# Kernel tuning notes

Hardware: AMD Instinct MI355X
Metric: run time of the kernel (lower is better)

## Reference

```python
import jax, jax.numpy as jnp
import numpy as np

B, S, D, H, L = 128, 200, 512, 512, 2  # batch, seq(=max_seq_len), input, hidden, layers


def _uni(key, shape, fan):
    bound = 1.0 / np.sqrt(fan)
    return jax.random.uniform(key, shape, jnp.float32, -bound, bound)


def setup_inputs() -> dict:
    key = jax.random.key(0)
    ks = jax.random.split(key, 12)
    x = jax.random.normal(ks[0], (B, S, D), jnp.float32)
    lens = jax.random.randint(ks[1], (B,), 1, S + 1).astype(jnp.int64)
    return {
        'x': x,
        'lens': lens,
        'Wih_f': _uni(ks[2], (L, 4 * H, D), H),
        'Whh_f': _uni(ks[3], (L, 4 * H, H), H),
        'bih_f': _uni(ks[4], (L, 4 * H), H),
        'bhh_f': _uni(ks[5], (L, 4 * H), H),
        'Wih_b': _uni(ks[6], (L, 4 * H, D), H),
        'Whh_b': _uni(ks[7], (L, 4 * H, H), H),
        'bih_b': _uni(ks[8], (L, 4 * H), H),
        'bhh_b': _uni(ks[9], (L, 4 * H), H),
    }


def _lstm_dir(xs, Wih, Whh, bih, bhh, reverse):
    # xs: [B,S,Din]. Precompute batched input projection, scan the recurrence.
    gx = jnp.einsum('bsd,gd->bsg', xs, Wih) + bih  # [B,S,4H]
    h0 = jnp.zeros((xs.shape[0], Whh.shape[1]), xs.dtype)
    c0 = jnp.zeros_like(h0)

    def step(carry, g_t):
        h, c = carry
        gates = g_t + h @ Whh.T + bhh
        i, f, g, o = jnp.split(gates, 4, axis=-1)  # PyTorch LSTMCell order
        i = jax.nn.sigmoid(i)
        f = jax.nn.sigmoid(f)
        g = jnp.tanh(g)
        o = jax.nn.sigmoid(o)
        c = f * c + i * g
        h = o * jnp.tanh(c)
        return (h, c), h

    _, hs = jax.lax.scan(step, (h0, c0), jnp.swapaxes(gx, 0, 1), reverse=reverse)
    return jnp.swapaxes(hs, 0, 1)  # [B,S,H], time-ordered


def reference(x, lens, Wih_f, Whh_f, bih_f, bhh_f, Wih_b, Whh_b, bih_b, bhh_b):
    valid = (jnp.arange(S)[None, :] < lens[:, None]).astype(x.dtype)[..., None]  # [B,S,1]
    f_in, b_in = x, x
    for l in range(L):
        f_h = _lstm_dir(f_in, Wih_f[l], Whh_f[l], bih_f[l], bhh_f[l], reverse=False)
        b_h = _lstm_dir(b_in, Wih_b[l], Whh_b[l], bih_b[l], bhh_b[l], reverse=True)
        f_h = f_h * valid  # masked_fill(mask, 0) for positions >= lens
        b_h = b_h * valid
        f_in, b_in = f_h, b_h
    return jnp.concatenate((f_in, b_in), axis=2)  # [B,S,2H]
```

## Files before the change

kernel.cpp:

```cpp
#include <hip/hip_runtime.h>
#include <hip/hip_bf16.h>

typedef __bf16 bf16x8 __attribute__((ext_vector_type(8)));
typedef _Float16 f16x8 __attribute__((ext_vector_type(8)));
typedef float f32x4 __attribute__((ext_vector_type(4)));

__device__ __forceinline__ unsigned short f2bf(float f) {
    unsigned int u = __builtin_bit_cast(unsigned int, f);
    u += 0x7FFFu + ((u >> 16) & 1u);
    return (unsigned short)(u >> 16);
}
__device__ __forceinline__ float bf2f(unsigned short s) {
    unsigned int u = ((unsigned int)s) << 16;
    return __builtin_bit_cast(float, u);
}

__device__ __forceinline__ void ldg_c(uint4& d, const void* p) {
    asm volatile("global_load_dwordx4 %0, %1, off sc0 sc1" : "=v"(d) : "v"(p));
}
__device__ __forceinline__ void stg_c32(void* p, unsigned v) {
    asm volatile("global_store_dword %0, %1, off sc0 sc1" :: "v"(p), "v"(v) : "memory");
}
__device__ __forceinline__ void vm_drain() {
    asm volatile("s_waitcnt vmcnt(0)" ::: "memory");
    __builtin_amdgcn_sched_barrier(0);
}
__device__ __forceinline__ void vm_wait_imm(int n) {
    switch (n) {
    case 0:  asm volatile("s_waitcnt vmcnt(0)"  ::: "memory"); break;
    case 4:  asm volatile("s_waitcnt vmcnt(4)"  ::: "memory"); break;
    case 8:  asm volatile("s_waitcnt vmcnt(8)"  ::: "memory"); break;
    case 12: asm volatile("s_waitcnt vmcnt(12)" ::: "memory"); break;
    case 16: asm volatile("s_waitcnt vmcnt(16)" ::: "memory"); break;
    case 20: asm volatile("s_waitcnt vmcnt(20)" ::: "memory"); break;
    case 24: asm volatile("s_waitcnt vmcnt(24)" ::: "memory"); break;
    default: asm volatile("s_waitcnt vmcnt(28)" ::: "memory"); break;
    }
    __builtin_amdgcn_sched_barrier(0);
}
__device__ __forceinline__ void lds_fence() {
    asm volatile("s_waitcnt lgkmcnt(0)" ::: "memory");
    __builtin_amdgcn_sched_barrier(0);
}

__device__ __forceinline__ void wait_flags(const unsigned* f, unsigned tgt) {
    int lane = threadIdx.x & 63;
    for (;;) {
        unsigned v = __hip_atomic_load(f + lane, __ATOMIC_RELAXED, __HIP_MEMORY_SCOPE_AGENT);
        if (__all((int)(v >= tgt))) break;
        __builtin_amdgcn_s_sleep(1);
    }
}

__global__ void prep_x(const float* __restrict__ x,
                       unsigned short* __restrict__ xh,
                       unsigned short* __restrict__ xl) {
    int g = blockIdx.x * 256 + threadIdx.x;
    if (g >= 1638400) return;
    int lane = g & 63;
    int kc   = (g >> 6) & 15;
    int nt   = (g >> 10) & 7;
    int t    = g >> 13;
    int batch = nt * 16 + (lane & 15);
    int k = kc * 32 + (lane >> 4) * 8;
    const float* s = x + ((size_t)batch * 200 + t) * 512 + k;
    float4 v0 = *(const float4*)s;
    float4 v1 = *(const float4*)(s + 4);
    float vv[8] = {v0.x, v0.y, v0.z, v0.w, v1.x, v1.y, v1.z, v1.w};
    unsigned int ph[4], pl[4];
    #pragma unroll
    for (int j = 0; j < 4; ++j) {
        float a = vv[2*j], b = vv[2*j+1];
        unsigned short ha = f2bf(a), hb = f2bf(b);
        unsigned short la = f2bf(a - bf2f(ha)), lb = f2bf(b - bf2f(hb));
        ph[j] = (unsigned)ha | ((unsigned)hb << 16);
        pl[j] = (unsigned)la | ((unsigned)lb << 16);
    }
    ((uint4*)xh)[g] = make_uint4(ph[0], ph[1], ph[2], ph[3]);
    ((uint4*)xl)[g] = make_uint4(pl[0], pl[1], pl[2], pl[3]);
}

__global__ void prep_w(const float* __restrict__ W,
                       unsigned short* __restrict__ wprep,
                       int dir, int isHH) {
    int g = blockIdx.x * 256 + threadIdx.x;
    if (g >= 262144) return;
    int lane = g & 63;
    int kc   = (g >> 6) & 15;
    int mt   = (g >> 10) & 1;
    int cu   = (g >> 11) & 63;
    int l    = g >> 17;
    int r = lane & 15;
    int grow = (2 * mt + (r >> 3)) * 512 + cu * 8 + (r & 7);
    int k = kc * 32 + (lane >> 4) * 8;
    const float* s = W + ((size_t)l * 2048 + grow) * 512 + k;
    float4 v0 = *(const float4*)s;
    float4 v1 = *(const float4*)(s + 4);
    float vv[8] = {v0.x, v0.y, v0.z, v0.w, v1.x, v1.y, v1.z, v1.w};
    bool f16fmt = isHH || (l == 1);
    unsigned int ph[4], pl[4];
    #pragma unroll
    for (int j = 0; j < 4; ++j) {
        float a = vv[2*j], b = vv[2*j+1];
        unsigned short ha, hb, la, lb;
        if (f16fmt) {
            _Float16 fa = (_Float16)a, fb = (_Float16)b;
            _Float16 ra = (_Float16)(a - (float)fa), rb = (_Float16)(b - (float)fb);
            ha = __builtin_bit_cast(unsigned short, fa);
            hb = __builtin_bit_cast(unsigned short, fb);
            la = __builtin_bit_cast(unsigned short, ra);
            lb = __builtin_bit_cast(unsigned short, rb);
        } else {
            ha = f2bf(a); hb = f2bf(b);
            la = f2bf(a - bf2f(ha)); lb = f2bf(b - bf2f(hb));
        }
        ph[j] = (unsigned)ha | ((unsigned)hb << 16);
        pl[j] = (unsigned)la | ((unsigned)lb << 16);
    }
    size_t blk = ((size_t)(dir * 2 + l) * 64 + cu) * 8192;
    size_t fH = blk + (size_t)((isHH * 2 + 0) * 2048 + mt * 1024 + kc * 64 + lane);
    size_t fL = blk + (size_t)((isHH * 2 + 1) * 2048 + mt * 1024 + kc * 64 + lane);
    ((uint4*)wprep)[fH] = make_uint4(ph[0], ph[1], ph[2], ph[3]);
    ((uint4*)wprep)[fL] = make_uint4(pl[0], pl[1], pl[2], pl[3]);
}

__global__ void bsum_k(const float* __restrict__ bih_f, const float* __restrict__ bhh_f,
                       const float* __restrict__ bih_b, const float* __restrict__ bhh_b,
                       float* __restrict__ bsum) {
    int i = blockIdx.x * 256 + threadIdx.x;
    if (i < 8192) {
        int dir = i >> 12, rem = i & 4095;
        const float* bi = dir ? bih_b : bih_f;
        const float* bh = dir ? bhh_b : bhh_f;
        bsum[i] = bi[rem] + bh[rem];
    }
}

__global__ void reset_k(uint4* __restrict__ p) {
    int g = blockIdx.x * 256 + threadIdx.x;
    if (g < 131136) p[g] = make_uint4(0, 0, 0, 0);
}

__global__ void __launch_bounds__(512)
lstm_persist(const unsigned short* __restrict__ xh,
             const unsigned short* __restrict__ xl,
             const unsigned short* __restrict__ wprep,
             const float*          __restrict__ bsum,
             unsigned short*       __restrict__ hbuf,
             const int*            __restrict__ lens,
             float*                __restrict__ dout,
             unsigned*             __restrict__ flagv)
{
    extern __shared__ char smem[];
    float* wexch  = (float*)(smem + 131072);
    float* cst    = (float*)(smem + 131072 + 17408);
    float* bias_l = (float*)(smem + 131072 + 17408 + 4224);

    const int bid  = blockIdx.x;
    const int xcd  = bid & 7;
    const int unit = xcd >> 1;
    const int slot = unit >> 1, dir = unit & 1;
    const int cu8  = ((xcd & 1) << 5) | (bid >> 3);
    const int hj0  = cu8 * 8;
    const int tid  = threadIdx.x;
    const int lane = tid & 63, ng = tid >> 6;
    const int l15  = lane & 15, kg = lane >> 4;
    const int wsel = dir * 2 + slot;

    const int sib = slot ? dir : (2 + dir);
    unsigned* own_f = flagv + unit * 64;
    unsigned* sib_f = flagv + sib * 64;

    {
        const uint4* src = (const uint4*)wprep + ((size_t)(wsel * 64 + cu8) * 8192);
        uint4* dst = (uint4*)smem;
        #pragma unroll
        for (int i = 0; i < 16; ++i) dst[tid + i * 512] = src[tid + i * 512];
    }
    for (int i = tid; i < 8 * 132; i += 512) cst[i] = 0.f;
    if (tid < 32) bias_l[tid] = bsum[wsel * 2048 + (tid >> 3) * 512 + hj0 + (tid & 7)];
    __syncthreads();

    const int lenv = lens[ng * 16 + l15];
    const int gb   = ng * 16 + l15;
    const int u0   = kg * 2;
    const size_t lofs = (size_t)lane * 8;
    const size_t hoff = ((size_t)(ng * 16 + (cu8 >> 2)) * 64 + (cu8 & 3) * 16 + l15) * 8 + u0;
    float* wex = wexch + ng * 32 * 17;

    for (int tau = 0; tau <= 200; ++tau) {
        const int t = slot ? (tau - 1) : tau;
        const bool active = (t >= 0 && t <= 199);
        int t_eff = 0, p_w = 0, p_r = 0;
        if (active) { t_eff = dir ? (199 - t) : t; p_w = t & 3; p_r = (t + 3) & 3; }

        f32x4 acc0 = {0.f, 0.f, 0.f, 0.f};
        f32x4 acc1 = {0.f, 0.f, 0.f, 0.f};

        unsigned probe = 0u;
        if (slot == 0 && ng == 0)
            probe = __hip_atomic_load(own_f + lane, __ATOMIC_RELAXED, __HIP_MEMORY_SCOPE_AGENT);

        if (slot == 0 && active) {
            const unsigned short* XH = xh + (size_t)t_eff * 65536;
            const unsigned short* XL = xl + (size_t)t_eff * 65536;
            #pragma unroll
            for (int kc = 0; kc < 16; ++kc) {
                size_t bo = (size_t)ng * 8192 + (size_t)kc * 512 + lofs;
                bf16x8 bxh = *(const bf16x8*)(XH + bo);
                bf16x8 bxl = *(const bf16x8*)(XL + bo);
                const char* ab = smem + kc * 1024 + lane * 16;
                bf16x8 aih0 = *(const bf16x8*)(ab);
                bf16x8 ail0 = *(const bf16x8*)(ab + 32768);
                bf16x8 aih1 = *(const bf16x8*)(ab + 16384);
                bf16x8 ail1 = *(const bf16x8*)(ab + 16384 + 32768);
                acc0 = __builtin_amdgcn_mfma_f32_16x16x32_bf16(aih0, bxh, acc0, 0, 0, 0);
                acc0 = __builtin_amdgcn_mfma_f32_16x16x32_bf16(aih0, bxl, acc0, 0, 0, 0);
                acc0 = __builtin_amdgcn_mfma_f32_16x16x32_bf16(ail0, bxh, acc0, 0, 0, 0);
                acc1 = __builtin_amdgcn_mfma_f32_16x16x32_bf16(aih1, bxh, acc1, 0, 0, 0);
                acc1 = __builtin_amdgcn_mfma_f32_16x16x32_bf16(aih1, bxl, acc1, 0, 0, 0);
                acc1 = __builtin_amdgcn_mfma_f32_16x16x32_bf16(ail1, bxh, acc1, 0, 0, 0);
            }
        }

        if (slot == 0) {
            if (ng == 0 && !__all((int)(probe >= (unsigned)tau)))
                wait_flags(own_f, (unsigned)tau);
            if (ng == 1 && tau >= 3) wait_flags(sib_f, (unsigned)(tau - 2));
        } else {
            if (ng == 0) wait_flags(own_f, (unsigned)tau);
            if (ng == 1) wait_flags(sib_f, (unsigned)tau);
        }
        __syncthreads();

        if (active) {
            const unsigned short* HH = hbuf + ((size_t)((slot * 4 + p_r) * 2 + dir) << 16);

            if (slot == 0) {
                uint4 vh[16];
                #pragma unroll
                for (int kc = 0; kc < 16; ++kc)
                    ldg_c(vh[kc], HH + (size_t)ng * 8192 + (size_t)kc * 512 + lofs);
                #pragma unroll
                for (int g = 0; g < 4; ++g) {
                    vm_wait_imm(12 - 4 * g);
                    #pragma unroll
                    for (int k2 = 0; k2 < 4; ++k2) {
                        int kc = g * 4 + k2;
                        f16x8 bh = __builtin_bit_cast(f16x8, vh[kc]);
                        const char* ab = smem + kc * 1024 + lane * 16;
                        f16x8 ahh0 = *(const f16x8*)(ab + 65536);
                        f16x8 ahl0 = *(const f16x8*)(ab + 98304);
                        f16x8 ahh1 = *(const f16x8*)(ab + 16384 + 65536);
                        f16x8 ahl1 = *(const f16x8*)(ab + 16384 + 98304);
                        acc0 = __builtin_amdgcn_mfma_f32_16x16x32_f16(ahh0, bh, acc0, 0, 0, 0);
                        acc0 = __builtin_amdgcn_mfma_f32_16x16x32_f16(ahl0, bh, acc0, 0, 0, 0);
                        acc1 = __builtin_amdgcn_mfma_f32_16x16x32_f16(ahh1, bh, acc1, 0, 0, 0);
                        acc1 = __builtin_amdgcn_mfma_f32_16x16x32_f16(ahl1, bh, acc1, 0, 0, 0);
                    }
                }
            } else {
                int p_x = t & 3;
                const unsigned short* XHc = hbuf + ((size_t)(p_x * 2 + dir) << 16);
                uint4 vh[16], vx[16];
                #pragma unroll
                for (int kc = 0; kc < 16; ++kc)
                    ldg_c(vh[kc], HH + (size_t)ng * 8192 + (size_t)kc * 512 + lofs);
                #pragma unroll
                for (int kc = 0; kc < 16; ++kc)
                    ldg_c(vx[kc], XHc + (size_t)ng * 8192 + (size_t)kc * 512 + lofs);
                #pragma unroll
                for (int g = 0; g < 4; ++g) {
                    vm_wait_imm(28 - 4 * g);
                    #pragma unroll
                    for (int k2 = 0; k2 < 4; ++k2) {
                        int kc = g * 4 + k2;
                        f16x8 bh = __builtin_bit_cast(f16x8, vh[kc]);
                        const char* ab = smem + kc * 1024 + lane * 16;
                        f16x8 ahh0 = *(const f16x8*)(ab + 65536);
                        f16x8 ahl0 = *(const f16x8*)(ab + 98304);
                        f16x8 ahh1 = *(const f16x8*)(ab + 16384 + 65536);
                        f16x8 ahl1 = *(const f16x8*)(ab + 16384 + 98304);
                        acc0 = __builtin_amdgcn_mfma_f32_16x16x32_f16(ahh0, bh, acc0, 0, 0, 0);
                        acc0 = __builtin_amdgcn_mfma_f32_16x16x32_f16(ahl0, bh, acc0, 0, 0, 0);
                        acc1 = __builtin_amdgcn_mfma_f32_16x16x32_f16(ahh1, bh, acc1, 0, 0, 0);
                        acc1 = __builtin_amdgcn_mfma_f32_16x16x32_f16(ahl1, bh, acc1, 0, 0, 0);
                    }
                }
                const bool mv = (t_eff < lenv);
                #pragma unroll
                for (int g = 0; g < 4; ++g) {
                    vm_wait_imm(12 - 4 * g);
                    #pragma unroll
                    for (int k2 = 0; k2 < 4; ++k2) {
                        int kc = g * 4 + k2;
                        if (!mv) vx[kc] = make_uint4(0, 0, 0, 0);
                        f16x8 xv = __builtin_bit_cast(f16x8, vx[kc]);
                        const char* ab = smem + kc * 1024 + lane * 16;
                        f16x8 aih0 = *(const f16x8*)(ab);
                        f16x8 aih1 = *(const f16x8*)(ab + 16384);
                        acc0 = __builtin_amdgcn_mfma_f32_16x16x32_f16(aih0, xv, acc0, 0, 0, 0);
                        acc1 = __builtin_amdgcn_mfma_f32_16x16x32_f16(aih1, xv, acc1, 0, 0, 0);
                    }
                }
            }

            #pragma unroll
            for (int r = 0; r < 4; ++r) {
                wex[(kg * 4 + r) * 17 + l15]      = acc0[r];
                wex[(16 + kg * 4 + r) * 17 + l15] = acc1[r];
            }
            lds_fence();

            unsigned short* Hw = hbuf + ((size_t)((slot * 4 + p_w) * 2 + dir) << 16);
            unsigned hpk = 0;
            float hm0 = 0.f, hm1 = 0.f;
            #pragma unroll
            for (int j = 0; j < 2; ++j) {
                int u = u0 + j;
                float g0 = wex[(0  + u) * 17 + l15] + bias_l[u];
                float g1 = wex[(8  + u) * 17 + l15] + bias_l[8 + u];
                float g2 = wex[(16 + u) * 17 + l15] + bias_l[16 + u];
                float g3 = wex[(24 + u) * 17 + l15] + bias_l[24 + u];
                float cv = cst[u * 132 + gb];
                float iG = 1.f / (1.f + expf(-g0));
                float fG = 1.f / (1.f + expf(-g1));
                float gG = tanhf(g2);
                float oG = 1.f / (1.f + expf(-g3));
                float cn = fG * cv + iG * gG;
                cst[u * 132 + gb] = cn;
                float hn = oG * tanhf(cn);
                _Float16 hf = (_Float16)hn;
                hpk |= ((unsigned)__builtin_bit_cast(unsigned short, hf)) << (16 * j);
                float hm = (t_eff < lenv) ? hn : 0.f;
                if (j) hm1 = hm; else hm0 = hm;
            }
            stg_c32(Hw + hoff, hpk);
            if (slot) {
                float2 o = make_float2(hm0, hm1);
                *(float2*)(dout + ((size_t)gb * 200 + t_eff) * 1024 + dir * 512 + hj0 + u0) = o;
            }
            vm_drain();
        }

        __syncthreads();
        if (tid == 0)
            __hip_atomic_store(own_f + cu8, (unsigned)(tau + 1),
                               __ATOMIC_RELAXED, __HIP_MEMORY_SCOPE_AGENT);
    }
}

extern "C" void kernel_launch(void* const* d_in, const int* in_sizes, int n_in,
                              void* d_out, int out_size, void* d_ws, size_t ws_size,
                              hipStream_t stream) {
    const float* x     = (const float*)d_in[0];
    const int*   lens  = (const int*)d_in[1];
    const float* Wih_f = (const float*)d_in[2];
    const float* Whh_f = (const float*)d_in[3];
    const float* bih_f = (const float*)d_in[4];
    const float* bhh_f = (const float*)d_in[5];
    const float* Wih_b = (const float*)d_in[6];
    const float* Whh_b = (const float*)d_in[7];
    const float* bih_b = (const float*)d_in[8];
    const float* bhh_b = (const float*)d_in[9];
    float* out = (float*)d_out;
    char* ws = (char*)d_ws;
    if (ws_size < 88114176) return;

    unsigned short* xh    = (unsigned short*)(ws);
    unsigned short* xl    = (unsigned short*)(ws + 26214400);
    unsigned short* wprep = (unsigned short*)(ws + 52428800);
    float*          bsum  = (float*)(ws + 85983232);
    unsigned short* hbuf  = (unsigned short*)(ws + 86016000);
    unsigned*       flg   = (unsigned*)(ws + 88113152);

    prep_x<<<6400, 256, 0, stream>>>(x, xh, xl);
    prep_w<<<1024, 256, 0, stream>>>(Wih_f, wprep, 0, 0);
    prep_w<<<1024, 256, 0, stream>>>(Whh_f, wprep, 0, 1);
    prep_w<<<1024, 256, 0, stream>>>(Wih_b, wprep, 1, 0);
    prep_w<<<1024, 256, 0, stream>>>(Whh_b, wprep, 1, 1);
    bsum_k<<<32, 256, 0, stream>>>(bih_f, bhh_f, bih_b, bhh_b, bsum);
    reset_k<<<513, 256, 0, stream>>>((uint4*)hbuf);

    static const int LDS_BYTES = 131072 + 17408 + 4224 + 128;
    hipFuncSetAttribute(reinterpret_cast<const void*>(lstm_persist),
                        hipFuncAttributeMaxDynamicSharedMemorySize, LDS_BYTES);

    void* args[] = {(void*)&xh, (void*)&xl, (void*)&wprep, (void*)&bsum,
                    (void*)&hbuf, (void*)&lens, (void*)&out, (void*)&flg};
    hipLaunchCooperativeKernel(reinterpret_cast<void*>(lstm_persist),
                               dim3(256), dim3(512), args, LDS_BYTES, stream);
}
```

Baseline: 1.837 ms.

## Replace block-wide barriers with per-wave flag synchronization in persistent LSTM

Each wave now owns its own set of progress flags, one per unit and wave, and waits only on the flags of the batch slice it reads. This removes the per-step __syncthreads and lets waves proceed independently. The sibling-slot wait in layer 0 moves to just before the h store, and layer 1 now waits for layer-0 output only after finishing its recurrent matmul. The staged vmcnt waits are replaced with full drains, which simplifies the code but loses the overlap of loads with MFMA work.

```diff
diff --git a/kernel.cpp b/kernel.cpp
--- a/kernel.cpp
+++ b/kernel.cpp
@@ -23,19 +23,6 @@
 }
 __device__ __forceinline__ void vm_drain() {
     asm volatile("s_waitcnt vmcnt(0)" ::: "memory");
-    __builtin_amdgcn_sched_barrier(0);
-}
-__device__ __forceinline__ void vm_wait_imm(int n) {
-    switch (n) {
-    case 0:  asm volatile("s_waitcnt vmcnt(0)"  ::: "memory"); break;
-    case 4:  asm volatile("s_waitcnt vmcnt(4)"  ::: "memory"); break;
-    case 8:  asm volatile("s_waitcnt vmcnt(8)"  ::: "memory"); break;
-    case 12: asm volatile("s_waitcnt vmcnt(12)" ::: "memory"); break;
-    case 16: asm volatile("s_waitcnt vmcnt(16)" ::: "memory"); break;
-    case 20: asm volatile("s_waitcnt vmcnt(20)" ::: "memory"); break;
-    case 24: asm volatile("s_waitcnt vmcnt(24)" ::: "memory"); break;
-    default: asm volatile("s_waitcnt vmcnt(28)" ::: "memory"); break;
-    }
     __builtin_amdgcn_sched_barrier(0);
 }
 __device__ __forceinline__ void lds_fence() {
@@ -138,7 +125,7 @@
 
 __global__ void reset_k(uint4* __restrict__ p) {
     int g = blockIdx.x * 256 + threadIdx.x;
-    if (g < 131136) p[g] = make_uint4(0, 0, 0, 0);
+    if (g < 131584) p[g] = make_uint4(0, 0, 0, 0);
 }
 
 __global__ void __launch_bounds__(512)
@@ -168,8 +155,8 @@
     const int wsel = dir * 2 + slot;
 
     const int sib = slot ? dir : (2 + dir);
-    unsigned* own_f = flagv + unit * 64;
-    unsigned* sib_f = flagv + sib * 64;
+    unsigned* own_f = flagv + (unit * 8 + ng) * 64;
+    unsigned* sib_f = flagv + (sib  * 8 + ng) * 64;
 
     {
         const uint4* src = (const uint4*)wprep + ((size_t)(wsel * 64 + cu8) * 8192);
@@ -191,117 +178,91 @@
     for (int tau = 0; tau <= 200; ++tau) {
         const int t = slot ? (tau - 1) : tau;
         const bool active = (t >= 0 && t <= 199);
-        int t_eff = 0, p_w = 0, p_r = 0;
-        if (active) { t_eff = dir ? (199 - t) : t; p_w = t & 3; p_r = (t + 3) & 3; }
-
-        f32x4 acc0 = {0.f, 0.f, 0.f, 0.f};
-        f32x4 acc1 = {0.f, 0.f, 0.f, 0.f};
-
-        unsigned probe = 0u;
-        if (slot == 0 && ng == 0)
-            probe = __hip_atomic_load(own_f + lane, __ATOMIC_RELAXED, __HIP_MEMORY_SCOPE_AGENT);
-
-        if (slot == 0 && active) {
-            const unsigned short* XH = xh + (size_t)t_eff * 65536;
-            const unsigned short* XL = xl + (size_t)t_eff * 65536;
-            #pragma unroll
-            for (int kc = 0; kc < 16; ++kc) {
-                size_t bo = (size_t)ng * 8192 + (size_t)kc * 512 + lofs;
-                bf16x8 bxh = *(const bf16x8*)(XH + bo);
-                bf16x8 bxl = *(const bf16x8*)(XL + bo);
-                const char* ab = smem + kc * 1024 + lane * 16;
-                bf16x8 aih0 = *(const bf16x8*)(ab);
-                bf16x8 ail0 = *(const bf16x8*)(ab + 32768);
-                bf16x8 aih1 = *(const bf16x8*)(ab + 16384);
-                bf16x8 ail1 = *(const bf16x8*)(ab + 16384 + 32768);
-                acc0 = __builtin_amdgcn_mfma_f32_16x16x32_bf16(aih0, bxh, acc0, 0, 0, 0);
-                acc0 = __builtin_amdgcn_mfma_f32_16x16x32_bf16(aih0, bxl, acc0, 0, 0, 0);
-                acc0 = __builtin_amdgcn_mfma_f32_16x16x32_bf16(ail0, bxh, acc0, 0, 0, 0);
-                acc1 = __builtin_amdgcn_mfma_f32_16x16x32_bf16(aih1, bxh, acc1, 0, 0, 0);
-                acc1 = __builtin_amdgcn_mfma_f32_16x16x32_bf16(aih1, bxl, acc1, 0, 0, 0);
-                acc1 = __builtin_amdgcn_mfma_f32_16x16x32_bf16(ail1, bxh, acc1, 0, 0, 0);
-            }
-        }
-
-        if (slot == 0) {
-            if (ng == 0 && !__all((int)(probe >= (unsigned)tau)))
+        if (active) {
+            const int t_eff = dir ? (199 - t) : t;
+            const int p_w = t & 3, p_r = (t + 3) & 3;
+            const unsigned short* HH = hbuf + ((size_t)((slot * 4 + p_r) * 2 + dir) << 16);
+
+            f32x4 acc0 = {0.f, 0.f, 0.f, 0.f};
+            f32x4 acc1 = {0.f, 0.f, 0.f, 0.f};
+
+            if (slot == 0) {
+                const unsigned short* XH = xh + (size_t)t_eff * 65536;
+                const unsigned short* XL = xl + (size_t)t_eff * 65536;
+                #pragma unroll
+                for (int kc = 0; kc < 16; ++kc) {
+                    size_t bo = (size_t)ng * 8192 + (size_t)kc * 512 + lofs;
+                    bf16x8 bxh = *(const bf16x8*)(XH + bo);
+                    bf16x8 bxl = *(const bf16x8*)(XL + bo);
+                    const char* ab = smem + kc * 1024 + lane * 16;
+                    bf16x8 aih0 = *(const bf16x8*)(ab);
+                    bf16x8 ail0 = *(const bf16x8*)(ab + 32768);
+                    bf16x8 aih1 = *(const bf16x8*)(ab + 16384);
+                    bf16x8 ail1 = *(const bf16x8*)(ab + 16384 + 32768);
+                    acc0 = __builtin_amdgcn_mfma_f32_16x16x32_bf16(aih0, bxh, acc0, 0, 0, 0);
+                    acc0 = __builtin_amdgcn_mfma_f32_16x16x32_bf16(aih0, bxl, acc0, 0, 0, 0);
+                    acc0 = __builtin_amdgcn_mfma_f32_16x16x32_bf16(ail0, bxh, acc0, 0, 0, 0);
+                    acc1 = __builtin_amdgcn_mfma_f32_16x16x32_bf16(aih1, bxh, acc1, 0, 0, 0);
+                    acc1 = __builtin_amdgcn_mfma_f32_16x16x32_bf16(aih1, bxl, acc1, 0, 0, 0);
+                    acc1 = __builtin_amdgcn_mfma_f32_16x16x32_bf16(ail1, bxh, acc1, 0, 0, 0);
+                }
                 wait_flags(own_f, (unsigned)tau);
-            if (ng == 1 && tau >= 3) wait_flags(sib_f, (unsigned)(tau - 2));
-        } else {
-            if (ng == 0) wait_flags(own_f, (unsigned)tau);
-            if (ng == 1) wait_flags(sib_f, (unsigned)tau);
-        }
-        __syncthreads();
-
-        if (active) {
-            const unsigned short* HH = hbuf + ((size_t)((slot * 4 + p_r) * 2 + dir) << 16);
-
-            if (slot == 0) {
                 uint4 vh[16];
                 #pragma unroll
                 for (int kc = 0; kc < 16; ++kc)
                     ldg_c(vh[kc], HH + (size_t)ng * 8192 + (size_t)kc * 512 + lofs);
-                #pragma unroll
-                for (int g = 0; g < 4; ++g) {
-                    vm_wait_imm(12 - 4 * g);
-                    #pragma unroll
-                    for (int k2 = 0; k2 < 4; ++k2) {
-                        int kc = g * 4 + k2;
-                        f16x8 bh = __builtin_bit_cast(f16x8, vh[kc]);
-                        const char* ab = smem + kc * 1024 + lane * 16;
-                        f16x8 ahh0 = *(const f16x8*)(ab + 65536);
-                        f16x8 ahl0 = *(const f16x8*)(ab + 98304);
-                        f16x8 ahh1 = *(const f16x8*)(ab + 16384 + 65536);
-                        f16x8 ahl1 = *(const f16x8*)(ab + 16384 + 98304);
-                        acc0 = __builtin_amdgcn_mfma_f32_16x16x32_f16(ahh0, bh, acc0, 0, 0, 0);
-                        acc0 = __builtin_amdgcn_mfma_f32_16x16x32_f16(ahl0, bh, acc0, 0, 0, 0);
-                        acc1 = __builtin_amdgcn_mfma_f32_16x16x32_f16(ahh1, bh, acc1, 0, 0, 0);
-                        acc1 = __builtin_amdgcn_mfma_f32_16x16x32_f16(ahl1, bh, acc1, 0, 0, 0);
-                    }
+                vm_drain();
+                #pragma unroll
+                for (int kc = 0; kc < 16; ++kc) {
+                    f16x8 bh = __builtin_bit_cast(f16x8, vh[kc]);
+                    const char* ab = smem + kc * 1024 + lane * 16;
+                    f16x8 ahh0 = *(const f16x8*)(ab + 65536);
+                    f16x8 ahl0 = *(const f16x8*)(ab + 98304);
+                    f16x8 ahh1 = *(const f16x8*)(ab + 16384 + 65536);
+                    f16x8 ahl1 = *(const f16x8*)(ab + 16384 + 98304);
+                    acc0 = __builtin_amdgcn_mfma_f32_16x16x32_f16(ahh0, bh, acc0, 0, 0, 0);
+                    acc0 = __builtin_amdgcn_mfma_f32_16x16x32_f16(ahl0, bh, acc0, 0, 0, 0);
+                    acc1 = __builtin_amdgcn_mfma_f32_16x16x32_f16(ahh1, bh, acc1, 0, 0, 0);
+                    acc1 = __builtin_amdgcn_mfma_f32_16x16x32_f16(ahl1, bh, acc1, 0, 0, 0);
                 }
             } else {
-                int p_x = t & 3;
-                const unsigned short* XHc = hbuf + ((size_t)(p_x * 2 + dir) << 16);
-                uint4 vh[16], vx[16];
+                wait_flags(own_f, (unsigned)tau);
+                uint4 vh[16];
                 #pragma unroll
                 for (int kc = 0; kc < 16; ++kc)
                     ldg_c(vh[kc], HH + (size_t)ng * 8192 + (size_t)kc * 512 + lofs);
+                vm_drain();
+                #pragma unroll
+                for (int kc = 0; kc < 16; ++kc) {
+                    f16x8 bh = __builtin_bit_cast(f16x8, vh[kc]);
+                    const char* ab = smem + kc * 1024 + lane * 16;
+                    f16x8 ahh0 = *(const f16x8*)(ab + 65536);
+                    f16x8 ahl0 = *(const f16x8*)(ab + 98304);
+                    f16x8 ahh1 = *(const f16x8*)(ab + 16384 + 65536);
+                    f16x8 ahl1 = *(const f16x8*)(ab + 16384 + 98304);
+                    acc0 = __builtin_amdgcn_mfma_f32_16x16x32_f16(ahh0, bh, acc0, 0, 0, 0);
+                    acc0 = __builtin_amdgcn_mfma_f32_16x16x32_f16(ahl0, bh, acc0, 0, 0, 0);
+                    acc1 = __builtin_amdgcn_mfma_f32_16x16x32_f16(ahh1, bh, acc1, 0, 0, 0);
+                    acc1 = __builtin_amdgcn_mfma_f32_16x16x32_f16(ahl1, bh, acc1, 0, 0, 0);
+                }
+                wait_flags(sib_f, (unsigned)tau);
+                const int p_x = t & 3;
+                const unsigned short* XHc = hbuf + ((size_t)(p_x * 2 + dir) << 16);
+                uint4 vx[16];
                 #pragma unroll
                 for (int kc = 0; kc < 16; ++kc)
                     ldg_c(vx[kc], XHc + (size_t)ng * 8192 + (size_t)kc * 512 + lofs);
-                #pragma unroll
-                for (int g = 0; g < 4; ++g) {
-                    vm_wait_imm(28 - 4 * g);
-                    #pragma unroll
-                    for (int k2 = 0; k2 < 4; ++k2) {
-                        int kc = g * 4 + k2;
-                        f16x8 bh = __builtin_bit_cast(f16x8, vh[kc]);
-                        const char* ab = smem + kc * 1024 + lane * 16;
-                        f16x8 ahh0 = *(const f16x8*)(ab + 65536);
-                        f16x8 ahl0 = *(const f16x8*)(ab + 98304);
-                        f16x8 ahh1 = *(const f16x8*)(ab + 16384 + 65536);
-                        f16x8 ahl1 = *(const f16x8*)(ab + 16384 + 98304);
-                        acc0 = __builtin_amdgcn_mfma_f32_16x16x32_f16(ahh0, bh, acc0, 0, 0, 0);
-                        acc0 = __builtin_amdgcn_mfma_f32_16x16x32_f16(ahl0, bh, acc0, 0, 0, 0);
-                        acc1 = __builtin_amdgcn_mfma_f32_16x16x32_f16(ahh1, bh, acc1, 0, 0, 0);
-                        acc1 = __builtin_amdgcn_mfma_f32_16x16x32_f16(ahl1, bh, acc1, 0, 0, 0);
-                    }
-                }
+                vm_drain();
                 const bool mv = (t_eff < lenv);
                 #pragma unroll
-                for (int g = 0; g < 4; ++g) {
-                    vm_wait_imm(12 - 4 * g);
-                    #pragma unroll
-                    for (int k2 = 0; k2 < 4; ++k2) {
-                        int kc = g * 4 + k2;
-                        if (!mv) vx[kc] = make_uint4(0, 0, 0, 0);
-                        f16x8 xv = __builtin_bit_cast(f16x8, vx[kc]);
-                        const char* ab = smem + kc * 1024 + lane * 16;
-                        f16x8 aih0 = *(const f16x8*)(ab);
-                        f16x8 aih1 = *(const f16x8*)(ab + 16384);
-                        acc0 = __builtin_amdgcn_mfma_f32_16x16x32_f16(aih0, xv, acc0, 0, 0, 0);
-                        acc1 = __builtin_amdgcn_mfma_f32_16x16x32_f16(aih1, xv, acc1, 0, 0, 0);
-                    }
+                for (int kc = 0; kc < 16; ++kc) {
+                    if (!mv) vx[kc] = make_uint4(0, 0, 0, 0);
+                    f16x8 xv = __builtin_bit_cast(f16x8, vx[kc]);
+                    const char* ab = smem + kc * 1024 + lane * 16;
+                    f16x8 aih0 = *(const f16x8*)(ab);
+                    f16x8 aih1 = *(const f16x8*)(ab + 16384);
+                    acc0 = __builtin_amdgcn_mfma_f32_16x16x32_f16(aih0, xv, acc0, 0, 0, 0);
+                    acc1 = __builtin_amdgcn_mfma_f32_16x16x32_f16(aih1, xv, acc1, 0, 0, 0);
                 }
             }
 
@@ -335,6 +296,7 @@
                 float hm = (t_eff < lenv) ? hn : 0.f;
                 if (j) hm1 = hm; else hm0 = hm;
             }
+            if (slot == 0 && tau >= 3) wait_flags(sib_f, (unsigned)(tau - 2));
             stg_c32(Hw + hoff, hpk);
             if (slot) {
                 float2 o = make_float2(hm0, hm1);
@@ -343,8 +305,7 @@
             vm_drain();
         }
 
-        __syncthreads();
-        if (tid == 0)
+        if (lane == 0)
             __hip_atomic_store(own_f + cu8, (unsigned)(tau + 1),
                                __ATOMIC_RELAXED, __HIP_MEMORY_SCOPE_AGENT);
     }
@@ -365,7 +326,7 @@
     const float* bhh_b = (const float*)d_in[9];
     float* out = (float*)d_out;
     char* ws = (char*)d_ws;
-    if (ws_size < 88114176) return;
+    if (ws_size < 88121344) return;
 
     unsigned short* xh    = (unsigned short*)(ws);
     unsigned short* xl    = (unsigned short*)(ws + 26214400);
@@ -380,7 +341,7 @@
     prep_w<<<1024, 256, 0, stream>>>(Wih_b, wprep, 1, 0);
     prep_w<<<1024, 256, 0, stream>>>(Whh_b, wprep, 1, 1);
     bsum_k<<<32, 256, 0, stream>>>(bih_f, bhh_f, bih_b, bhh_b, bsum);
-    reset_k<<<513, 256, 0, stream>>>((uint4*)hbuf);
+    reset_k<<<514, 256, 0, stream>>>((uint4*)hbuf);
 
     static const int LDS_BYTES = 131072 + 17408 + 4224 + 128;
     hipFuncSetAttribute(reinterpret_cast<const void*>(lstm_persist),
```

Result: slower. 4.735 ms (+157.8%).
